# Kernel optimization log

Measured on AMD Instinct MI355X. Metric: run time of the kernel, lower is better.

## Reference

```python
import jax, jax.numpy as jnp
import numpy as np

# --- static config (matches init_kwargs) ---
B = 2048
N_UP, N_DOWN, N_NUC = 16, 14, 8
N_ELEC = N_UP + N_DOWN            # 30
N_ALL = N_ELEC + N_NUC            # 38
BASIS, KD, ED, L = 32, 64, 128, 3
H_K = int(np.round(np.sqrt(BASIS * KD)))  # 45, log-interp hidden dim of kernel MLP
H_O = int(np.round(np.sqrt(KD * ED)))     # 91, log-interp hidden dim of embed_out MLP

# conv_indexing: all (i, j) pairs with j != i  (i over electrons, j over all particles)
_pairs = np.array([(i, j) for i in range(N_ELEC) for j in range(N_ALL) if j != i], dtype=np.int32)
C_I = jnp.asarray(_pairs[:, 0])
C_J = jnp.asarray(_pairs[:, 1])
P = N_ELEC * (N_ALL - 1)


def ssp(x):
    # shifted softplus: log(0.5*exp(x) + 0.5)
    return jax.nn.softplus(x) - jnp.log(2.0).astype(x.dtype)


def setup_inputs() -> dict:
    key = jax.random.key(0)
    ks = jax.random.split(key, 16)
    # spin-shared electron embeddings (one vector per spin channel, expanded)
    up = jax.random.normal(ks[0], (ED,), jnp.float32)
    dn = jax.random.normal(ks[1], (ED,), jnp.float32)
    embedding_elec = jnp.concatenate([jnp.tile(up, (N_UP, 1)), jnp.tile(dn, (N_DOWN, 1))], axis=0)
    s = 0.1  # weight scale for numerical sanity
    inp = {
        'dists_basis': jax.random.uniform(ks[2], (B, N_ELEC, N_ALL, BASIS), jnp.float32),
        'embedding_elec': embedding_elec,
        'embedding_nuc': jax.random.normal(ks[3], (N_NUC, KD), jnp.float32),
        'kernel_w1': s * jax.random.normal(ks[4], (L, BASIS, H_K), jnp.float32),
        'kernel_b1': s * jax.random.normal(ks[5], (L, H_K), jnp.float32),
        'kernel_w2': s * jax.random.normal(ks[6], (L, H_K, KD), jnp.float32),
        'kernel_b2': s * jax.random.normal(ks[7], (L, KD), jnp.float32),
        'embed_in_w': s * jax.random.normal(ks[8], (L, ED, KD), jnp.float32),
        'out_w1': s * jax.random.normal(ks[9], (L, KD, H_O), jnp.float32),
        'out_b1': s * jax.random.normal(ks[10], (L, H_O), jnp.float32),
        'out_w2': s * jax.random.normal(ks[11], (L, H_O, ED), jnp.float32),
        'out_b2': s * jax.random.normal(ks[12], (L, ED), jnp.float32),
    }
    return inp


def reference(dists_basis, embedding_elec, embedding_nuc, kernel_w1, kernel_b1,
              kernel_w2, kernel_b2, embed_in_w, out_w1, out_b1, out_w2, out_b2):
    b = dists_basis.shape[0]
    # gather all (i,j) pair basis features: (B, P, BASIS)
    db = dists_basis[:, C_I, C_J, :]
    xs = jnp.broadcast_to(embedding_elec, (b, N_ELEC, ED))
    nuc = jnp.broadcast_to(embedding_nuc, (b, N_NUC, KD))
    for l in range(L):  # small fixed number of interaction layers
        # kernel MLP on distance basis -> (B, P, KD)
        Ws = ssp(db @ kernel_w1[l] + kernel_b1[l]) @ kernel_w2[l] + kernel_b2[l]
        # embed_in on electrons, concat nuclei embeddings -> (B, N_ALL, KD)
        zs = jnp.concatenate([xs @ embed_in_w[l], nuc], axis=1)
        # gather neighbors, weight, reduce over neighbor axis -> (B, N_ELEC, KD)
        msg = (Ws * zs[:, C_J]).reshape(b, N_ELEC, N_ALL - 1, KD).sum(axis=2)
        # embed_out MLP -> (B, N_ELEC, ED), residual update
        vs = ssp(msg @ out_w1[l] + out_b1[l]) @ out_w2[l] + out_b2[l]
        xs = xs + vs
    return xs
```

## Files before the change

### kernel.cpp

```cpp
#include <hip/hip_runtime.h>
#include <hip/hip_bf16.h>

typedef __attribute__((ext_vector_type(8))) short bf16x8;
typedef __attribute__((ext_vector_type(4))) float f32x4;

constexpr int NB = 2048;
constexpr int NE = 30, NN = 8, NAll = 38;
constexpr int BAS = 32, KD = 64, ED = 128, HK = 45, HO = 91, LNUM = 3;

__device__ __forceinline__ unsigned short f2b(float v) {
    __hip_bfloat16 h = __float2bfloat16(v);
    return __builtin_bit_cast(unsigned short, h);
}
__device__ __forceinline__ float ssp(float x) {
    float e = __expf(-fabsf(x));
    return fmaxf(x, 0.f) + __logf(1.f + e) - 0.69314718055994530942f;
}
__device__ __forceinline__ int swzi(int row, int col, int S) {
    int mask = (S >> 3) - 1;
    int blk = ((col >> 3) ^ row) & mask;
    return row * S + (blk << 3) + (col & 7);
}
__device__ __forceinline__ bf16x8 ldfrag(const unsigned short* p, int S, int row, int col) {
    int mask = (S >> 3) - 1;
    int blk = ((col >> 3) ^ row) & mask;
    return *(const bf16x8*)(p + row * S + (blk << 3));
}
__device__ __forceinline__ f32x4 ldf4s(const float* p, int S, int row, int col) {
    int mask = (S >> 3) - 1;
    int blk = ((col >> 3) ^ row) & mask;
    return *(const f32x4*)(p + row * S + (blk << 3) + (col & 7));
}
__device__ __forceinline__ bf16x8 cvt8(f32x4 lo, f32x4 hi) {
    bf16x8 r;
    r[0] = (short)f2b(lo[0]); r[1] = (short)f2b(lo[1]);
    r[2] = (short)f2b(lo[2]); r[3] = (short)f2b(lo[3]);
    r[4] = (short)f2b(hi[0]); r[5] = (short)f2b(hi[1]);
    r[6] = (short)f2b(hi[2]); r[7] = (short)f2b(hi[3]);
    return r;
}

__global__ __launch_bounds__(256, 4) void schnet_mfma(
    const float* __restrict__ dists,
    const float* __restrict__ emb_e,
    const float* __restrict__ emb_n,
    const float* __restrict__ kw1, const float* __restrict__ kb1,
    const float* __restrict__ kw2, const float* __restrict__ kb2,
    const float* __restrict__ ew,
    const float* __restrict__ ow1, const float* __restrict__ ob1,
    const float* __restrict__ ow2, const float* __restrict__ ob2,
    float* __restrict__ out)
{
    __shared__ __align__(16) unsigned char smem[38656];
    float* zsb  = (float*)smem;
    float* stot = (float*)(smem + 9728);
    unsigned char* U = smem + 9984;

    const int b = blockIdx.x;
    const int t = threadIdx.x;
    const int lane = t & 63, wv = t >> 6;
    const int q = lane >> 4, cc = lane & 15;
    const float* db_b = dists + (size_t)b * NE * NAll * BAS;
    float* xsg = out + (size_t)b * NE * ED;

    const f32x4 zz = {0.f, 0.f, 0.f, 0.f};

    for (int o = t; o < NE * ED; o += 256) xsg[o] = emb_e[o];
    for (int o = t; o < NN * KD; o += 256) zsb[NE * KD + o] = emb_n[o];
    __syncthreads();

    for (int l = 0; l < LNUM; ++l) {
        const float* w1g = kw1 + l * BAS * HK;
        const float* b1g = kb1 + l * HK;
        const float* w2g = kw2 + l * HK * KD;
        const float* b2g = kb2 + l * KD;
        const float* weg = ew  + l * ED * KD;
        const float* o1g = ow1 + l * KD * HO;
        const float* g1g = ob1 + l * HO;
        const float* o2g = ow2 + l * ED * 0 + l * HO * ED;
        const float* g2g = ob2 + l * ED;

        {
            unsigned short* wet = (unsigned short*)U;
            for (int o = t; o < 64 * 128; o += 256) {
                int k = o & 63, e = o >> 6;
                wet[swzi(k, e, 128)] = f2b(weg[e * 64 + k]);
            }
            __syncthreads();
            #pragma unroll
            for (int mt = 0; mt < 2; ++mt) {
                const int row = mt * 16 + cc;
                const bool va = (row < NE);
                f32x4 acc = zz;
                #pragma unroll
                for (int ks = 0; ks < 4; ++ks) {
                    bf16x8 a = {0, 0, 0, 0, 0, 0, 0, 0};
                    if (va) {
                        const float* p = xsg + row * ED + ks * 32 + q * 8;
                        a = cvt8(*(const f32x4*)p, *(const f32x4*)(p + 4));
                    }
                    acc = __builtin_amdgcn_mfma_f32_16x16x32_bf16(
                        a, ldfrag(wet, 128, wv * 16 + cc, ks * 32 + q * 8), acc, 0, 0, 0);
                }
                #pragma unroll
                for (int r = 0; r < 4; ++r) {
                    int rr = mt * 16 + q * 4 + r;
                    if (rr < NE) zsb[rr * 64 + wv * 16 + cc] = acc[r];
                }
            }
            __syncthreads();
        }

        unsigned short* w1t = (unsigned short*)U;
        unsigned short* w2t = (unsigned short*)(U + 3072);
        if (t < 64) {
            float s = 0.f;
            for (int jj = 0; jj < NAll; ++jj) s += zsb[jj * 64 + t];
            stot[t] = s;
        }
        for (int o = t; o < 48 * 32; o += 256) {
            int h = o % 48, e = o / 48;
            float v = (h < HK) ? w1g[e * HK + h] : 0.f;
            w1t[swzi(h, e, 32)] = f2b(v);
        }
        for (int o = t; o < 64 * 64; o += 256) {
            int c2 = o & 63, h = o >> 6;
            float v = (h < HK) ? w2g[h * KD + c2] : 0.f;
            w2t[swzi(c2, h, 64)] = f2b(v);
        }
        __syncthreads();

        bf16x8 w1f[3], w2f[4][2];
        float b1v[3];
        #pragma unroll
        for (int nt = 0; nt < 3; ++nt) {
            w1f[nt] = ldfrag(w1t, 32, nt * 16 + cc, q * 8);
            int col = nt * 16 + cc;
            b1v[nt] = (col < HK) ? b1g[col] : 0.f;
        }
        #pragma unroll
        for (int nt = 0; nt < 4; ++nt) {
            w2f[nt][0] = ldfrag(w2t, 64, nt * 16 + cc, q * 8);
            w2f[nt][1] = ldfrag(w2t, 64, nt * 16 + cc, 32 + q * 8);
        }
        __syncthreads();

        unsigned short* Hb = (unsigned short*)(U + wv * 4096);
        {
            f32x4* hz = (f32x4*)Hb;
            for (int o = lane; o < 256; o += 64) hz[o] = zz;
        }
        f32x4 mr[2][4];
        #pragma unroll
        for (int mt = 0; mt < 2; ++mt)
            #pragma unroll
            for (int nt = 0; nt < 4; ++nt) mr[mt][nt] = zz;

        for (int j = wv; j < NAll; j += 4) {
            const float* dp0 = db_b + (cc * NAll + j) * BAS + q * 8;
            bf16x8 fa0 = cvt8(*(const f32x4*)dp0, *(const f32x4*)(dp0 + 4));
            bf16x8 fa1 = {0, 0, 0, 0, 0, 0, 0, 0};
            if (cc < NE - 16) {
                const float* dp1 = dp0 + 16 * NAll * BAS;
                fa1 = cvt8(*(const f32x4*)dp1, *(const f32x4*)(dp1 + 4));
            }
            #pragma unroll
            for (int nt = 0; nt < 3; ++nt) {
                f32x4 h0 = __builtin_amdgcn_mfma_f32_16x16x32_bf16(fa0, w1f[nt], zz, 0, 0, 0);
                f32x4 h1 = __builtin_amdgcn_mfma_f32_16x16x32_bf16(fa1, w1f[nt], zz, 0, 0, 0);
                int col = nt * 16 + cc;
                float bb = b1v[nt];
                #pragma unroll
                for (int r = 0; r < 4; ++r) {
                    Hb[swzi(q * 4 + r, col, 64)]      = f2b(ssp(h0[r] + bb));
                    Hb[swzi(16 + q * 4 + r, col, 64)] = f2b(ssp(h1[r] + bb));
                }
            }
            float zv[4];
            #pragma unroll
            for (int nt = 0; nt < 4; ++nt) zv[nt] = zsb[j * 64 + nt * 16 + cc];
            #pragma unroll
            for (int mt = 0; mt < 2; ++mt) {
                bf16x8 afA = ldfrag(Hb, 64, mt * 16 + cc, q * 8);
                bf16x8 afB = ldfrag(Hb, 64, mt * 16 + cc, 32 + q * 8);
                #pragma unroll
                for (int nt = 0; nt < 4; ++nt) {
                    f32x4 acc = __builtin_amdgcn_mfma_f32_16x16x32_bf16(afA, w2f[nt][0], zz, 0, 0, 0);
                    acc = __builtin_amdgcn_mfma_f32_16x16x32_bf16(afB, w2f[nt][1], acc, 0, 0, 0);
                    #pragma unroll
                    for (int r = 0; r < 4; ++r) {
                        int ii = mt * 16 + q * 4 + r;
                        if (ii < NE && j != ii) mr[mt][nt][r] += acc[r] * zv[nt];
                    }
                }
            }
        }
        __syncthreads();

        float* msgf0 = (float*)U;
        float* msgf1 = (float*)(U + 8192);
        if (wv < 2) {
            float* dst = wv ? msgf1 : msgf0;
            #pragma unroll
            for (int mt = 0; mt < 2; ++mt)
                #pragma unroll
                for (int nt = 0; nt < 4; ++nt) {
                    int col = nt * 16 + cc;
                    #pragma unroll
                    for (int r = 0; r < 4; ++r) {
                        int i = mt * 16 + q * 4 + r;
                        float v = mr[mt][nt][r];
                        if (wv == 0 && i < NE)
                            v += b2g[col] * (stot[col] - zsb[i * 64 + col]);
                        dst[swzi(i, col, 64)] = v;
                    }
                }
        }
        __syncthreads();
        if (wv >= 2) {
            float* dst = (wv == 3) ? msgf1 : msgf0;
            #pragma unroll
            for (int mt = 0; mt < 2; ++mt)
                #pragma unroll
                for (int nt = 0; nt < 4; ++nt) {
                    int col = nt * 16 + cc;
                    #pragma unroll
                    for (int r = 0; r < 4; ++r)
                        dst[swzi(mt * 16 + q * 4 + r, col, 64)] += mr[mt][nt][r];
                }
        }
        __syncthreads();
        for (int o = t; o < 2048; o += 256) msgf0[o] += msgf1[o];
        __syncthreads();

        {
            unsigned short* o1t = (unsigned short*)(U + 8192);
            unsigned short* hob = (unsigned short*)(U + 20480);
            for (int o = t; o < 96 * 64; o += 256) {
                int h = o % 96, m = o / 96;
                float v = (h < HO) ? o1g[m * HO + h] : 0.f;
                o1t[swzi(h, m, 64)] = f2b(v);
            }
            __syncthreads();
            {
                const int mt = wv & 1;
                bf16x8 afo[2];
                #pragma unroll
                for (int ks = 0; ks < 2; ++ks) {
                    f32x4 p0 = ldf4s(msgf0, 64, mt * 16 + cc, ks * 32 + q * 8);
                    f32x4 p1 = ldf4s(msgf0, 64, mt * 16 + cc, ks * 32 + q * 8 + 4);
                    afo[ks] = cvt8(p0, p1);
                }
                #pragma unroll
                for (int s = 0; s < 3; ++s) {
                    int nt = (wv >> 1) + 2 * s;
                    f32x4 acc = __builtin_amdgcn_mfma_f32_16x16x32_bf16(
                        afo[0], ldfrag(o1t, 64, nt * 16 + cc, q * 8), zz, 0, 0, 0);
                    acc = __builtin_amdgcn_mfma_f32_16x16x32_bf16(
                        afo[1], ldfrag(o1t, 64, nt * 16 + cc, 32 + q * 8), acc, 0, 0, 0);
                    int col = nt * 16 + cc;
                    float g1v = (col < HO) ? g1g[col] : 0.f;
                    #pragma unroll
                    for (int r = 0; r < 4; ++r)
                        hob[swzi(mt * 16 + q * 4 + r, col, 128)] = f2b(ssp(acc[r] + g1v));
                }
            }
            __syncthreads();
            unsigned short* o2t = (unsigned short*)U;
            #pragma unroll
            for (int ph = 0; ph < 2; ++ph) {
                for (int o = t; o < 8192; o += 256) {
                    int e = o & 63, h = o >> 6;
                    float v = (h < HO) ? o2g[h * ED + ph * 64 + e] : 0.f;
                    o2t[swzi(e, h, 128)] = f2b(v);
                }
                __syncthreads();
                float g2v = g2g[ph * 64 + wv * 16 + cc];
                #pragma unroll
                for (int mt = 0; mt < 2; ++mt) {
                    f32x4 acc = zz;
                    #pragma unroll
                    for (int ks = 0; ks < 3; ++ks)
                        acc = __builtin_amdgcn_mfma_f32_16x16x32_bf16(
                            ldfrag(hob, 128, mt * 16 + cc, ks * 32 + q * 8),
                            ldfrag(o2t, 128, wv * 16 + cc, ks * 32 + q * 8), acc, 0, 0, 0);
                    #pragma unroll
                    for (int r = 0; r < 4; ++r) {
                        int i = mt * 16 + q * 4 + r;
                        if (i < NE) xsg[i * ED + ph * 64 + wv * 16 + cc] += acc[r] + g2v;
                    }
                }
                __syncthreads();
            }
        }
    }
}

extern "C" void kernel_launch(void* const* d_in, const int* in_sizes, int n_in,
                              void* d_out, int out_size, void* d_ws, size_t ws_size,
                              hipStream_t stream) {
    const float* dists = (const float*)d_in[0];
    const float* emb_e = (const float*)d_in[1];
    const float* emb_n = (const float*)d_in[2];
    const float* kw1   = (const float*)d_in[3];
    const float* kb1   = (const float*)d_in[4];
    const float* kw2   = (const float*)d_in[5];
    const float* kb2   = (const float*)d_in[6];
    const float* ew    = (const float*)d_in[7];
    const float* ow1   = (const float*)d_in[8];
    const float* ob1   = (const float*)d_in[9];
    const float* ow2   = (const float*)d_in[10];
    const float* ob2   = (const float*)d_in[11];
    float* out = (float*)d_out;

    schnet_mfma<<<NB, 256, 0, stream>>>(dists, emb_e, emb_n, kw1, kb1, kw2, kb2,
                                        ew, ow1, ob1, ow2, ob2, out);
}
```

Before: 1.386 ms.

## Shrink LDS footprint, split weight staging, and simplify pair loop masking

Cuts shared memory from about 38.6KB to 30KB and raises launch bounds occupancy from 4 to 5 blocks per CU. To fit, weight staging for embed_in, out_w1 and out_w2 is split into K halves with more barriers, and the hidden buffer is split into 32+16 column pieces. The per-pair i!=j mask is replaced by an unconditional accumulate plus a diagonal-correction pass run by wave 0. Cross-wave message reduction now uses LDS atomicAdd instead of staged buffers, and bf16 conversion uses packed v_cvt_pk_bf16_f32. The extra syncs and the serial diagonal pass on one wave may offset part of the occupancy benefit.

```diff
diff --git a/kernel.cpp b/kernel.cpp
--- a/kernel.cpp
+++ b/kernel.cpp
@@ -3,14 +3,29 @@
 
 typedef __attribute__((ext_vector_type(8))) short bf16x8;
 typedef __attribute__((ext_vector_type(4))) float f32x4;
+typedef __attribute__((ext_vector_type(2))) unsigned int u32x2;
 
 constexpr int NB = 2048;
 constexpr int NE = 30, NN = 8, NAll = 38;
 constexpr int BAS = 32, KD = 64, ED = 128, HK = 45, HO = 91, LNUM = 3;
 
+#define MFMA(a, b, c) __builtin_amdgcn_mfma_f32_16x16x32_bf16((a), (b), (c), 0, 0, 0)
+
+__device__ __forceinline__ unsigned cvtpk(float a, float b) {
+    unsigned r;
+    asm("v_cvt_pk_bf16_f32 %0, %1, %2" : "=v"(r) : "v"(a), "v"(b));
+    return r;
+}
 __device__ __forceinline__ unsigned short f2b(float v) {
-    __hip_bfloat16 h = __float2bfloat16(v);
-    return __builtin_bit_cast(unsigned short, h);
+    return (unsigned short)cvtpk(v, v);
+}
+__device__ __forceinline__ bf16x8 cvt8(f32x4 lo, f32x4 hi) {
+    union { unsigned u[4]; bf16x8 v; } r;
+    r.u[0] = cvtpk(lo[0], lo[1]);
+    r.u[1] = cvtpk(lo[2], lo[3]);
+    r.u[2] = cvtpk(hi[0], hi[1]);
+    r.u[3] = cvtpk(hi[2], hi[3]);
+    return r.v;
 }
 __device__ __forceinline__ float ssp(float x) {
     float e = __expf(-fabsf(x));
@@ -31,16 +46,8 @@
     int blk = ((col >> 3) ^ row) & mask;
     return *(const f32x4*)(p + row * S + (blk << 3) + (col & 7));
 }
-__device__ __forceinline__ bf16x8 cvt8(f32x4 lo, f32x4 hi) {
-    bf16x8 r;
-    r[0] = (short)f2b(lo[0]); r[1] = (short)f2b(lo[1]);
-    r[2] = (short)f2b(lo[2]); r[3] = (short)f2b(lo[3]);
-    r[4] = (short)f2b(hi[0]); r[5] = (short)f2b(hi[1]);
-    r[6] = (short)f2b(hi[2]); r[7] = (short)f2b(hi[3]);
-    return r;
-}
-
-__global__ __launch_bounds__(256, 4) void schnet_mfma(
+
+__global__ __launch_bounds__(256, 5) void schnet_mfma(
     const float* __restrict__ dists,
     const float* __restrict__ emb_e,
     const float* __restrict__ emb_n,
@@ -51,10 +58,12 @@
     const float* __restrict__ ow2, const float* __restrict__ ob2,
     float* __restrict__ out)
 {
-    __shared__ __align__(16) unsigned char smem[38656];
+    __shared__ __align__(16) unsigned char smem[30464];
     float* zsb  = (float*)smem;
     float* stot = (float*)(smem + 9728);
-    unsigned char* U = smem + 9984;
+    unsigned short* w2tA = (unsigned short*)(smem + 9984);
+    unsigned short* w2tB = (unsigned short*)(smem + 14080);
+    unsigned char* U = smem + 16128;
 
     const int b = blockIdx.x;
     const int t = threadIdx.x;
@@ -64,6 +73,7 @@
     float* xsg = out + (size_t)b * NE * ED;
 
     const f32x4 zz = {0.f, 0.f, 0.f, 0.f};
+    const bf16x8 zb = {0, 0, 0, 0, 0, 0, 0, 0};
 
     for (int o = t; o < NE * ED; o += 256) xsg[o] = emb_e[o];
     for (int o = t; o < NN * KD; o += 256) zsb[NE * KD + o] = emb_n[o];
@@ -77,217 +87,240 @@
         const float* weg = ew  + l * ED * KD;
         const float* o1g = ow1 + l * KD * HO;
         const float* g1g = ob1 + l * HO;
-        const float* o2g = ow2 + l * ED * 0 + l * HO * ED;
+        const float* o2g = ow2 + l * HO * ED;
         const float* g2g = ob2 + l * ED;
 
         {
             unsigned short* wet = (unsigned short*)U;
-            for (int o = t; o < 64 * 128; o += 256) {
-                int k = o & 63, e = o >> 6;
-                wet[swzi(k, e, 128)] = f2b(weg[e * 64 + k]);
-            }
-            __syncthreads();
-            #pragma unroll
-            for (int mt = 0; mt < 2; ++mt) {
-                const int row = mt * 16 + cc;
-                const bool va = (row < NE);
-                f32x4 acc = zz;
-                #pragma unroll
-                for (int ks = 0; ks < 4; ++ks) {
-                    bf16x8 a = {0, 0, 0, 0, 0, 0, 0, 0};
-                    if (va) {
-                        const float* p = xsg + row * ED + ks * 32 + q * 8;
-                        a = cvt8(*(const f32x4*)p, *(const f32x4*)(p + 4));
-                    }
-                    acc = __builtin_amdgcn_mfma_f32_16x16x32_bf16(
-                        a, ldfrag(wet, 128, wv * 16 + cc, ks * 32 + q * 8), acc, 0, 0, 0);
-                }
-                #pragma unroll
-                for (int r = 0; r < 4; ++r) {
-                    int rr = mt * 16 + q * 4 + r;
-                    if (rr < NE) zsb[rr * 64 + wv * 16 + cc] = acc[r];
-                }
-            }
-            __syncthreads();
-        }
-
-        unsigned short* w1t = (unsigned short*)U;
-        unsigned short* w2t = (unsigned short*)(U + 3072);
+            f32x4 zacc[2] = {zz, zz};
+            #pragma unroll
+            for (int kh = 0; kh < 2; ++kh) {
+                for (int o = t; o < 64 * 64; o += 256) {
+                    int c2 = o & 63, e2 = o >> 6;
+                    wet[swzi(c2, e2, 64)] = f2b(weg[(kh * 64 + e2) * KD + c2]);
+                }
+                if (kh == 0) {
+                    for (int o = t; o < 64 * 32; o += 256) {
+                        int c2 = o & 63, h = o >> 6;
+                        w2tA[swzi(c2, h, 32)] = f2b(w2g[h * KD + c2]);
+                    }
+                    for (int o = t; o < 64 * 16; o += 256) {
+                        int c2 = o & 63, h2 = o >> 6, h = 32 + h2;
+                        w2tB[swzi(c2, h2, 16)] = f2b((h < HK) ? w2g[h * KD + c2] : 0.f);
+                    }
+                }
+                __syncthreads();
+                #pragma unroll
+                for (int ksl = 0; ksl < 2; ++ksl) {
+                    bf16x8 wf = ldfrag(wet, 64, wv * 16 + cc, ksl * 32 + q * 8);
+                    #pragma unroll
+                    for (int mt = 0; mt < 2; ++mt) {
+                        int ra = mt * 16 + cc; if (ra > NE - 1) ra = NE - 1;
+                        const float* xp = xsg + ra * ED + kh * 64 + ksl * 32 + q * 8;
+                        zacc[mt] = MFMA(cvt8(*(const f32x4*)xp, *(const f32x4*)(xp + 4)), wf, zacc[mt]);
+                    }
+                }
+                if (kh == 1) {
+                    #pragma unroll
+                    for (int mt = 0; mt < 2; ++mt)
+                        #pragma unroll
+                        for (int r = 0; r < 4; ++r) {
+                            int rr = mt * 16 + q * 4 + r;
+                            if (rr < NE) zsb[rr * 64 + wv * 16 + cc] = zacc[mt][r];
+                        }
+                }
+                __syncthreads();
+            }
+        }
+
         if (t < 64) {
             float s = 0.f;
             for (int jj = 0; jj < NAll; ++jj) s += zsb[jj * 64 + t];
             stot[t] = s;
         }
-        for (int o = t; o < 48 * 32; o += 256) {
-            int h = o % 48, e = o / 48;
-            float v = (h < HK) ? w1g[e * HK + h] : 0.f;
-            w1t[swzi(h, e, 32)] = f2b(v);
-        }
-        for (int o = t; o < 64 * 64; o += 256) {
-            int c2 = o & 63, h = o >> 6;
-            float v = (h < HK) ? w2g[h * KD + c2] : 0.f;
-            w2t[swzi(c2, h, 64)] = f2b(v);
-        }
-        __syncthreads();
-
-        bf16x8 w1f[3], w2f[4][2];
-        float b1v[3];
+
+        bf16x8 w1f[3]; f32x4 b1q[3];
         #pragma unroll
         for (int nt = 0; nt < 3; ++nt) {
-            w1f[nt] = ldfrag(w1t, 32, nt * 16 + cc, q * 8);
-            int col = nt * 16 + cc;
-            b1v[nt] = (col < HK) ? b1g[col] : 0.f;
-        }
-        #pragma unroll
-        for (int nt = 0; nt < 4; ++nt) {
-            w2f[nt][0] = ldfrag(w2t, 64, nt * 16 + cc, q * 8);
-            w2f[nt][1] = ldfrag(w2t, 64, nt * 16 + cc, 32 + q * 8);
-        }
-        __syncthreads();
-
-        unsigned short* Hb = (unsigned short*)(U + wv * 4096);
-        {
-            f32x4* hz = (f32x4*)Hb;
-            for (int o = lane; o < 256; o += 64) hz[o] = zz;
-        }
+            int h = nt * 16 + cc;
+            if (h < HK) {
+                f32x4 lo, hi;
+                #pragma unroll
+                for (int jj = 0; jj < 4; ++jj) lo[jj] = w1g[(q * 8 + jj) * HK + h];
+                #pragma unroll
+                for (int jj = 0; jj < 4; ++jj) hi[jj] = w1g[(q * 8 + 4 + jj) * HK + h];
+                w1f[nt] = cvt8(lo, hi);
+            } else w1f[nt] = zb;
+            b1q[nt] = *(const f32x4*)(b1g + nt * 16 + q * 4);
+        }
+
+        unsigned short* HbA = (unsigned short*)(U + wv * 3072);
+        unsigned short* HbB = HbA + 1024;
         f32x4 mr[2][4];
         #pragma unroll
         for (int mt = 0; mt < 2; ++mt)
             #pragma unroll
             for (int nt = 0; nt < 4; ++nt) mr[mt][nt] = zz;
 
-        for (int j = wv; j < NAll; j += 4) {
-            const float* dp0 = db_b + (cc * NAll + j) * BAS + q * 8;
+        auto pbody = [&](bool DIAG, int j) {
+            int r1 = 16 + cc; if (r1 > NE - 1) r1 = NE - 1;
+            int j0 = DIAG ? cc : j;
+            int j1 = DIAG ? r1 : j;
+            const float* dp0 = db_b + (cc * NAll + j0) * BAS + q * 8;
+            const float* dp1 = db_b + (r1 * NAll + j1) * BAS + q * 8;
             bf16x8 fa0 = cvt8(*(const f32x4*)dp0, *(const f32x4*)(dp0 + 4));
-            bf16x8 fa1 = {0, 0, 0, 0, 0, 0, 0, 0};
-            if (cc < NE - 16) {
-                const float* dp1 = dp0 + 16 * NAll * BAS;
-                fa1 = cvt8(*(const f32x4*)dp1, *(const f32x4*)(dp1 + 4));
-            }
+            bf16x8 fa1 = cvt8(*(const f32x4*)dp1, *(const f32x4*)(dp1 + 4));
             #pragma unroll
             for (int nt = 0; nt < 3; ++nt) {
-                f32x4 h0 = __builtin_amdgcn_mfma_f32_16x16x32_bf16(fa0, w1f[nt], zz, 0, 0, 0);
-                f32x4 h1 = __builtin_amdgcn_mfma_f32_16x16x32_bf16(fa1, w1f[nt], zz, 0, 0, 0);
+                f32x4 h0 = MFMA(w1f[nt], fa0, zz);
+                f32x4 h1 = MFMA(w1f[nt], fa1, zz);
+                u32x2 v0, v1;
+                v0.x = cvtpk(ssp(h0[0] + b1q[nt][0]), ssp(h0[1] + b1q[nt][1]));
+                v0.y = cvtpk(ssp(h0[2] + b1q[nt][2]), ssp(h0[3] + b1q[nt][3]));
+                v1.x = cvtpk(ssp(h1[0] + b1q[nt][0]), ssp(h1[1] + b1q[nt][1]));
+                v1.y = cvtpk(ssp(h1[2] + b1q[nt][2]), ssp(h1[3] + b1q[nt][3]));
+                if (nt < 2) {
+                    *(u32x2*)(HbA + swzi(cc,      nt * 16 + q * 4, 32)) = v0;
+                    *(u32x2*)(HbA + swzi(16 + cc, nt * 16 + q * 4, 32)) = v1;
+                } else {
+                    *(u32x2*)(HbB + swzi(cc,      q * 4, 16)) = v0;
+                    *(u32x2*)(HbB + swzi(16 + cc, q * 4, 16)) = v1;
+                }
+            }
+            float zv[4];
+            if (!DIAG) {
+                #pragma unroll
+                for (int nt = 0; nt < 4; ++nt) zv[nt] = zsb[j * 64 + nt * 16 + cc];
+            }
+            bf16x8 afA[2], afB[2];
+            #pragma unroll
+            for (int mt = 0; mt < 2; ++mt) {
+                afA[mt] = ldfrag(HbA, 32, mt * 16 + cc, q * 8);
+                afB[mt] = ldfrag(HbB, 16, mt * 16 + cc, q * 8);
+                if (q >= 2) afB[mt] = zb;
+            }
+            #pragma unroll
+            for (int nt = 0; nt < 4; ++nt) {
+                bf16x8 wA = ldfrag(w2tA, 32, nt * 16 + cc, q * 8);
+                bf16x8 wB = ldfrag(w2tB, 16, nt * 16 + cc, q * 8);
+                #pragma unroll
+                for (int mt = 0; mt < 2; ++mt) {
+                    f32x4 a2 = MFMA(afA[mt], wA, zz);
+                    a2 = MFMA(afB[mt], wB, a2);
+                    #pragma unroll
+                    for (int r = 0; r < 4; ++r) {
+                        if (DIAG)
+                            mr[mt][nt][r] -= a2[r] * zsb[(mt * 16 + q * 4 + r) * 64 + nt * 16 + cc];
+                        else
+                            mr[mt][nt][r] += a2[r] * zv[nt];
+                    }
+                }
+            }
+        };
+
+        for (int j = wv; j < NAll; j += 4) pbody(false, j);
+        if (wv == 0) pbody(true, 0);
+        __syncthreads();
+
+        float* msgf = (float*)U;
+        #pragma unroll
+        for (int o = 0; o < 2; ++o) *(f32x4*)(msgf + t * 4 + o * 1024) = zz;
+        __syncthreads();
+        if (wv == 0) {
+            #pragma unroll
+            for (int nt = 0; nt < 4; ++nt) {
                 int col = nt * 16 + cc;
-                float bb = b1v[nt];
-                #pragma unroll
-                for (int r = 0; r < 4; ++r) {
-                    Hb[swzi(q * 4 + r, col, 64)]      = f2b(ssp(h0[r] + bb));
-                    Hb[swzi(16 + q * 4 + r, col, 64)] = f2b(ssp(h1[r] + bb));
-                }
-            }
-            float zv[4];
-            #pragma unroll
-            for (int nt = 0; nt < 4; ++nt) zv[nt] = zsb[j * 64 + nt * 16 + cc];
-            #pragma unroll
-            for (int mt = 0; mt < 2; ++mt) {
-                bf16x8 afA = ldfrag(Hb, 64, mt * 16 + cc, q * 8);
-                bf16x8 afB = ldfrag(Hb, 64, mt * 16 + cc, 32 + q * 8);
-                #pragma unroll
-                for (int nt = 0; nt < 4; ++nt) {
-                    f32x4 acc = __builtin_amdgcn_mfma_f32_16x16x32_bf16(afA, w2f[nt][0], zz, 0, 0, 0);
-                    acc = __builtin_amdgcn_mfma_f32_16x16x32_bf16(afB, w2f[nt][1], acc, 0, 0, 0);
-                    #pragma unroll
-                    for (int r = 0; r < 4; ++r) {
-                        int ii = mt * 16 + q * 4 + r;
-                        if (ii < NE && j != ii) mr[mt][nt][r] += acc[r] * zv[nt];
-                    }
-                }
-            }
-        }
+                float b2v = b2g[col];
+                float st = stot[col];
+                #pragma unroll
+                for (int mt = 0; mt < 2; ++mt)
+                    #pragma unroll
+                    for (int r = 0; r < 4; ++r)
+                        mr[mt][nt][r] += b2v * (st - zsb[(mt * 16 + q * 4 + r) * 64 + col]);
+            }
+        }
+        #pragma unroll
+        for (int mt = 0; mt < 2; ++mt)
+            #pragma unroll
+            for (int nt = 0; nt < 4; ++nt)
+                #pragma unroll
+                for (int r = 0; r < 4; ++r)
+                    atomicAdd(msgf + swzi(mt * 16 + q * 4 + r, nt * 16 + cc, 64), mr[mt][nt][r]);
         __syncthreads();
 
-        float* msgf0 = (float*)U;
-        float* msgf1 = (float*)(U + 8192);
-        if (wv < 2) {
-            float* dst = wv ? msgf1 : msgf0;
-            #pragma unroll
-            for (int mt = 0; mt < 2; ++mt)
-                #pragma unroll
-                for (int nt = 0; nt < 4; ++nt) {
-                    int col = nt * 16 + cc;
-                    #pragma unroll
-                    for (int r = 0; r < 4; ++r) {
-                        int i = mt * 16 + q * 4 + r;
-                        float v = mr[mt][nt][r];
-                        if (wv == 0 && i < NE)
-                            v += b2g[col] * (stot[col] - zsb[i * 64 + col]);
-                        dst[swzi(i, col, 64)] = v;
-                    }
-                }
-        }
-        __syncthreads();
-        if (wv >= 2) {
-            float* dst = (wv == 3) ? msgf1 : msgf0;
-            #pragma unroll
-            for (int mt = 0; mt < 2; ++mt)
-                #pragma unroll
-                for (int nt = 0; nt < 4; ++nt) {
-                    int col = nt * 16 + cc;
-                    #pragma unroll
-                    for (int r = 0; r < 4; ++r)
-                        dst[swzi(mt * 16 + q * 4 + r, col, 64)] += mr[mt][nt][r];
-                }
-        }
-        __syncthreads();
-        for (int o = t; o < 2048; o += 256) msgf0[o] += msgf1[o];
-        __syncthreads();
-
         {
-            unsigned short* o1t = (unsigned short*)(U + 8192);
-            unsigned short* hob = (unsigned short*)(U + 20480);
-            for (int o = t; o < 96 * 64; o += 256) {
-                int h = o % 96, m = o / 96;
-                float v = (h < HO) ? o1g[m * HO + h] : 0.f;
-                o1t[swzi(h, m, 64)] = f2b(v);
-            }
-            __syncthreads();
-            {
-                const int mt = wv & 1;
-                bf16x8 afo[2];
-                #pragma unroll
-                for (int ks = 0; ks < 2; ++ks) {
-                    f32x4 p0 = ldf4s(msgf0, 64, mt * 16 + cc, ks * 32 + q * 8);
-                    f32x4 p1 = ldf4s(msgf0, 64, mt * 16 + cc, ks * 32 + q * 8 + 4);
-                    afo[ks] = cvt8(p0, p1);
-                }
+            unsigned short* o1t  = (unsigned short*)(U + 8192);
+            unsigned short* hobA = (unsigned short*)U;
+            unsigned short* hobB = hobA + 2048;
+            const int ih = wv & 1;
+            bf16x8 afo[2];
+            #pragma unroll
+            for (int ks = 0; ks < 2; ++ks)
+                afo[ks] = cvt8(ldf4s(msgf, 64, ih * 16 + cc, ks * 32 + q * 8),
+                               ldf4s(msgf, 64, ih * 16 + cc, ks * 32 + q * 8 + 4));
+            f32x4 oa[3] = {zz, zz, zz};
+            #pragma unroll
+            for (int kh = 0; kh < 2; ++kh) {
+                for (int o = t; o < 96 * 32; o += 256) {
+                    int h = o % 96, m = o / 96;
+                    o1t[swzi(h, m, 32)] = f2b((h < HO) ? o1g[(kh * 32 + m) * HO + h] : 0.f);
+                }
+                __syncthreads();
                 #pragma unroll
                 for (int s = 0; s < 3; ++s) {
-                    int nt = (wv >> 1) + 2 * s;
-                    f32x4 acc = __builtin_amdgcn_mfma_f32_16x16x32_bf16(
-                        afo[0], ldfrag(o1t, 64, nt * 16 + cc, q * 8), zz, 0, 0, 0);
-                    acc = __builtin_amdgcn_mfma_f32_16x16x32_bf16(
-                        afo[1], ldfrag(o1t, 64, nt * 16 + cc, 32 + q * 8), acc, 0, 0, 0);
-                    int col = nt * 16 + cc;
-                    float g1v = (col < HO) ? g1g[col] : 0.f;
-                    #pragma unroll
-                    for (int r = 0; r < 4; ++r)
-                        hob[swzi(mt * 16 + q * 4 + r, col, 128)] = f2b(ssp(acc[r] + g1v));
-                }
-            }
-            __syncthreads();
-            unsigned short* o2t = (unsigned short*)U;
+                    int ht = (wv >> 1) + 2 * s;
+                    oa[s] = MFMA(ldfrag(o1t, 32, ht * 16 + cc, q * 8), afo[kh], oa[s]);
+                }
+                if (kh == 1) {
+                    #pragma unroll
+                    for (int s = 0; s < 3; ++s) {
+                        int ht = (wv >> 1) + 2 * s;
+                        f32x4 g1q = *(const f32x4*)(g1g + ht * 16 + q * 4);
+                        u32x2 hv;
+                        hv.x = cvtpk(ssp(oa[s][0] + g1q[0]), ssp(oa[s][1] + g1q[1]));
+                        hv.y = cvtpk(ssp(oa[s][2] + g1q[2]), ssp(oa[s][3] + g1q[3]));
+                        int i = ih * 16 + cc;
+                        if (ht < 4) *(u32x2*)(hobA + swzi(i, ht * 16 + q * 4, 64)) = hv;
+                        else        *(u32x2*)(hobB + swzi(i, (ht - 4) * 16 + q * 4, 32)) = hv;
+                    }
+                }
+                __syncthreads();
+            }
+            unsigned short* o2t = (unsigned short*)(U + 6144);
             #pragma unroll
             for (int ph = 0; ph < 2; ++ph) {
-                for (int o = t; o < 8192; o += 256) {
+                for (int o = t; o < 64 * 64; o += 256) {
                     int e = o & 63, h = o >> 6;
-                    float v = (h < HO) ? o2g[h * ED + ph * 64 + e] : 0.f;
-                    o2t[swzi(e, h, 128)] = f2b(v);
-                }
-                __syncthreads();
-                float g2v = g2g[ph * 64 + wv * 16 + cc];
-                #pragma unroll
-                for (int mt = 0; mt < 2; ++mt) {
-                    f32x4 acc = zz;
-                    #pragma unroll
-                    for (int ks = 0; ks < 3; ++ks)
-                        acc = __builtin_amdgcn_mfma_f32_16x16x32_bf16(
-                            ldfrag(hob, 128, mt * 16 + cc, ks * 32 + q * 8),
-                            ldfrag(o2t, 128, wv * 16 + cc, ks * 32 + q * 8), acc, 0, 0, 0);
-                    #pragma unroll
-                    for (int r = 0; r < 4; ++r) {
-                        int i = mt * 16 + q * 4 + r;
-                        if (i < NE) xsg[i * ED + ph * 64 + wv * 16 + cc] += acc[r] + g2v;
+                    o2t[swzi(e, h, 64)] = f2b(o2g[h * ED + ph * 64 + e]);
+                }
+                __syncthreads();
+                f32x4 acc2[2];
+                {
+                    bf16x8 bf0 = ldfrag(o2t, 64, wv * 16 + cc, q * 8);
+                    bf16x8 bf1 = ldfrag(o2t, 64, wv * 16 + cc, 32 + q * 8);
+                    #pragma unroll
+                    for (int mt = 0; mt < 2; ++mt) {
+                        acc2[mt] = MFMA(ldfrag(hobA, 64, mt * 16 + cc, q * 8), bf0, zz);
+                        acc2[mt] = MFMA(ldfrag(hobA, 64, mt * 16 + cc, 32 + q * 8), bf1, acc2[mt]);
+                    }
+                }
+                __syncthreads();
+                for (int o = t; o < 64 * 32; o += 256) {
+                    int e = o & 63, h2 = o >> 6, h = 64 + h2;
+                    o2t[swzi(e, h2, 32)] = f2b((h < HO) ? o2g[h * ED + ph * 64 + e] : 0.f);
+                }
+                __syncthreads();
+                {
+                    bf16x8 bf2 = ldfrag(o2t, 32, wv * 16 + cc, q * 8);
+                    float g2v = g2g[ph * 64 + wv * 16 + cc];
+                    #pragma unroll
+                    for (int mt = 0; mt < 2; ++mt) {
+                        acc2[mt] = MFMA(ldfrag(hobB, 32, mt * 16 + cc, q * 8), bf2, acc2[mt]);
+                        #pragma unroll
+                        for (int r = 0; r < 4; ++r) {
+                            int i = mt * 16 + q * 4 + r;
+                            if (i < NE) xsg[i * ED + ph * 64 + wv * 16 + cc] += acc2[mt][r] + g2v;
+                        }
                     }
                 }
                 __syncthreads();
```

New measurement: 1.459 ms. 5.3% more time.
